# Kernel tuning notes

Measured on AMD Instinct MI355X. Metric: run time of the kernel, lower is better.

Reference implementation:

```python
import jax, jax.numpy as jnp
import numpy as np

B, R, O, D = 32, 3136, 20, 32  # batch, rays(=56*56), objects, d_object
H = W = 56


def setup_inputs() -> dict:
    key = jax.random.key(0)
    k1, k2, k3 = jax.random.split(key, 3)
    form_decoding = jax.random.normal(k1, (B, R, O, D), dtype=jnp.float32)
    depth = jax.random.normal(k2, (B, R, O), dtype=jnp.float32)
    # original: transmitance = -t**2 (non-positive) so exp(transmitance) <= 1
    transmitance = -jax.random.uniform(k3, (B, R, O), dtype=jnp.float32)
    return {"form_decoding": form_decoding, "depth": depth, "transmitance": transmitance}


def reference(form_decoding, depth, transmitance):
    # NeRF-style alpha compositing over objects along each ray.
    o = depth.shape[-1]
    # pairwise depth comparison: sigmoid(1000*(D[...,o] - D[...,O])), zero diag
    diff = depth[..., :, None] - depth[..., None, :]              # [b,r,o,O]
    comp = jax.nn.sigmoid(1000.0 * diff) * (1.0 - jnp.eye(o, dtype=depth.dtype))
    # accumulated log-transmittance of objects in front
    acc = jnp.einsum('brO,broO->bro', transmitance, comp)         # [b,r,o]
    ponderation = jnp.exp(acc) * (1.0 - jnp.exp(transmitance))    # [b,r,o]
    result = jnp.einsum('bro,brod->brd', ponderation, form_decoding)  # [b,r,d]
    b = form_decoding.shape[0]
    result = result.reshape(b, H, W, -1).transpose(0, 3, 1, 2)    # [b,d,H,W]
    return (result, ponderation)
```

## Files before the change

### kernel.cpp

```cpp
#include <hip/hip_runtime.h>

#define NB 32
#define NR 3136
#define NO 20
#define ND 32
#define RAYS_PER_BLOCK 8

__global__ __launch_bounds__(256) void ray_composite(
    const float* __restrict__ form,
    const float* __restrict__ depth,
    const float* __restrict__ trans,
    float* __restrict__ out_res,
    float* __restrict__ out_pond)
{
  const int ray  = blockIdx.x * RAYS_PER_BLOCK + (threadIdx.x >> 5);
  const int lane = threadIdx.x & 31;
  const int b = ray / NR;
  const int r = ray - b * NR;

  const float* dep = depth + (size_t)ray * NO;
  const float* trs = trans + (size_t)ray * NO;

  float d_o = 0.0f, t_o = 0.0f;
  if (lane < NO) { d_o = dep[lane]; t_o = trs[lane]; }

  float acc = 0.0f;
#pragma unroll
  for (int j = 0; j < NO; ++j) {
    const float dj = __shfl(d_o, j, 32);
    const float tj = __shfl(t_o, j, 32);
    const float s  = 1.0f / (1.0f + __expf(-1000.0f * (d_o - dj)));
    if (j != lane) acc += tj * s;
  }

  float pond = __expf(acc) * (1.0f - __expf(t_o));
  if (lane >= NO) pond = 0.0f;
  if (lane < NO) out_pond[(size_t)ray * NO + lane] = pond;

  const float* f = form + (size_t)ray * (NO * ND);
  float res = 0.0f;
#pragma unroll
  for (int o = 0; o < NO; ++o) {
    const float p = __shfl(pond, o, 32);
    res += p * f[o * ND + lane];
  }

  out_res[(size_t)b * (ND * NR) + (size_t)lane * NR + r] = res;
}

extern "C" void kernel_launch(void* const* d_in, const int* in_sizes, int n_in,
                              void* d_out, int out_size, void* d_ws, size_t ws_size,
                              hipStream_t stream) {
  const float* form  = (const float*)d_in[0];
  const float* depth = (const float*)d_in[1];
  const float* trans = (const float*)d_in[2];

  float* out_res  = (float*)d_out;
  float* out_pond = out_res + (size_t)NB * ND * NR;

  const int nrays = NB * NR;
  dim3 grid(nrays / RAYS_PER_BLOCK);
  dim3 block(256);
  ray_composite<<<grid, block, 0, stream>>>(form, depth, trans, out_res, out_pond);
}
```

Before: 55.32 us.

## Vectorize form loads and stage outputs in LDS for coalesced transposed stores

```diff
diff --git a/kernel.cpp b/kernel.cpp
--- a/kernel.cpp
+++ b/kernel.cpp
@@ -4,48 +4,74 @@
 #define NR 3136
 #define NO 20
 #define ND 32
-#define RAYS_PER_BLOCK 8
+#define RPB 16
+#define BLOCK (RPB * 32)
 
-__global__ __launch_bounds__(256) void ray_composite(
+__global__ __launch_bounds__(BLOCK) void ray_composite(
     const float* __restrict__ form,
     const float* __restrict__ depth,
     const float* __restrict__ trans,
     float* __restrict__ out_res,
     float* __restrict__ out_pond)
 {
-  const int ray  = blockIdx.x * RAYS_PER_BLOCK + (threadIdx.x >> 5);
-  const int lane = threadIdx.x & 31;
-  const int b = ray / NR;
-  const int r = ray - b * NR;
+  __shared__ float res_lds[RPB][36];
+  __shared__ float pond_lds[RPB * NO];
 
-  const float* dep = depth + (size_t)ray * NO;
-  const float* trs = trans + (size_t)ray * NO;
+  const int t    = threadIdx.x;
+  const int rib  = t >> 5;
+  const int lane = t & 31;
+  const int ray0 = blockIdx.x * RPB;
+  const int ray  = ray0 + rib;
+  const int b    = ray0 / NR;
+  const int r0   = ray0 - b * NR;
 
-  float d_o = 0.0f, t_o = 0.0f;
-  if (lane < NO) { d_o = dep[lane]; t_o = trs[lane]; }
-
-  float acc = 0.0f;
+  float d_o = 0.f, t_o = 0.f;
+  if (lane < NO) {
+    d_o = depth[(size_t)ray * NO + lane];
+    t_o = trans[(size_t)ray * NO + lane];
+  }
+  float acc = 0.f;
 #pragma unroll
   for (int j = 0; j < NO; ++j) {
     const float dj = __shfl(d_o, j, 32);
     const float tj = __shfl(t_o, j, 32);
-    const float s  = 1.0f / (1.0f + __expf(-1000.0f * (d_o - dj)));
+    const float s  = 1.f / (1.f + __expf(-1000.f * (d_o - dj)));
     if (j != lane) acc += tj * s;
   }
+  float pond = __expf(acc) * (1.f - __expf(t_o));
+  if (lane >= NO) pond = 0.f;
+  if (lane < NO) pond_lds[rib * NO + lane] = pond;
 
-  float pond = __expf(acc) * (1.0f - __expf(t_o));
-  if (lane >= NO) pond = 0.0f;
-  if (lane < NO) out_pond[(size_t)ray * NO + lane] = pond;
+  const int c  = lane & 7;
+  const int og = lane >> 3;
+  const float* fbase = form + (size_t)ray * (NO * ND);
+  float4 accv = make_float4(0.f, 0.f, 0.f, 0.f);
+#pragma unroll
+  for (int k = 0; k < 5; ++k) {
+    const int o = og + 4 * k;
+    const float p = __shfl(pond, o, 32);
+    const float4 v = *reinterpret_cast<const float4*>(fbase + o * ND + c * 4);
+    accv.x += p * v.x; accv.y += p * v.y; accv.z += p * v.z; accv.w += p * v.w;
+  }
+#pragma unroll
+  for (int m = 8; m <= 16; m <<= 1) {
+    accv.x += __shfl_xor(accv.x, m, 32);
+    accv.y += __shfl_xor(accv.y, m, 32);
+    accv.z += __shfl_xor(accv.z, m, 32);
+    accv.w += __shfl_xor(accv.w, m, 32);
+  }
+  if (lane < 8)
+    *reinterpret_cast<float4*>(&res_lds[rib][lane * 4]) = accv;
 
-  const float* f = form + (size_t)ray * (NO * ND);
-  float res = 0.0f;
-#pragma unroll
-  for (int o = 0; o < NO; ++o) {
-    const float p = __shfl(pond, o, 32);
-    res += p * f[o * ND + lane];
+  __syncthreads();
+
+  {
+    const int d  = t >> 4;
+    const int rr = t & 15;
+    out_res[(size_t)b * (ND * NR) + (size_t)d * NR + r0 + rr] = res_lds[rr][d];
   }
-
-  out_res[(size_t)b * (ND * NR) + (size_t)lane * NR + r] = res;
+  if (t < RPB * NO)
+    out_pond[(size_t)ray0 * NO + t] = pond_lds[t];
 }
 
 extern "C" void kernel_launch(void* const* d_in, const int* in_sizes, int n_in,
@@ -58,8 +84,7 @@
   float* out_res  = (float*)d_out;
   float* out_pond = out_res + (size_t)NB * ND * NR;
 
-  const int nrays = NB * NR;
-  dim3 grid(nrays / RAYS_PER_BLOCK);
-  dim3 block(256);
+  dim3 grid((NB * NR) / RPB);
+  dim3 block(BLOCK);
   ray_composite<<<grid, block, 0, stream>>>(form, depth, trans, out_res, out_pond);
 }
```

Result: faster. 50.08 us (-9.5%).
